# Optimization experiments

Hardware: AMD Instinct MI355X
Metric: run time of the kernel (lower is better)

Reference implementation:

```python
import jax, jax.numpy as jnp
import numpy as np

B, N, D, H = 4, 4096, 1024, 16
HD = D // H


def setup_inputs() -> dict:
    key = jax.random.key(0)
    k_x, k_qkv, k_proj, k_b = jax.random.split(key, 4)
    x = jax.random.normal(k_x, (B, N, D), dtype=jnp.float32)
    # torch nn.Linear weights: (out_features, in_features)
    w_qkv = jax.random.normal(k_qkv, (3 * D, D), dtype=jnp.float32) * (D ** -0.5)
    w_proj = jax.random.normal(k_proj, (D, D), dtype=jnp.float32) * (D ** -0.5)
    b_proj = jax.random.normal(k_b, (D,), dtype=jnp.float32) * 0.01
    return {"x": x, "w_qkv": w_qkv, "w_proj": w_proj, "b_proj": b_proj}


def reference(x, w_qkv, w_proj, b_proj):
    b, n, d = x.shape
    # qkv projection (no bias, qkv_bias=False)
    qkv = x @ w_qkv.T                       # (b, n, 3d)
    qkv = qkv.reshape(b, n, 3, H, HD)
    q, k, v = qkv[:, :, 0], qkv[:, :, 1], qkv[:, :, 2]   # each (b, n, H, HD)
    # Faithful to source: q @ k.transpose(-2,-1) with q,k of shape (b,n,H,HD)
    # -> per-token (H,H) attention across heads, softmax over last (head) axis.
    scale = HD ** -0.5
    attn = jnp.einsum('bnhd,bngd->bnhg', q, k) * scale   # (b, n, H, H)
    attn = jax.nn.softmax(attn, axis=-1)
    o = jnp.einsum('bnhg,bngd->bnhd', attn, v)           # (b, n, H, HD)
    # source: transpose(1,2).reshape(b,n,d) (contiguous copy then reshape)
    o = jnp.swapaxes(o, 1, 2).reshape(b, n, d)
    return o @ w_proj.T + b_proj
```

## Files before the change

kernel.cpp:

```cpp
#include <hip/hip_runtime.h>
#include <hip/hip_bf16.h>
#include <cstdint>
#include <cstddef>

#define NB      4
#define NSEQ    4096
#define DM      1024
#define NTOK    16384
#define QKV_N   3072

typedef __attribute__((ext_vector_type(8))) short short8_t;
typedef __attribute__((ext_vector_type(4))) float f32x4;

static __device__ __forceinline__ unsigned short f2bf(float f) {
    unsigned u = __builtin_bit_cast(unsigned, f);
    u += 0x7fffu + ((u >> 16) & 1u);
    return (unsigned short)(u >> 16);
}

static __device__ __forceinline__ void async16(const void* g, void* l) {
    __builtin_amdgcn_global_load_lds(
        (const __attribute__((address_space(1))) void*)g,
        (__attribute__((address_space(3))) void*)l, 16, 0, 0);
}

__global__ void cvt_f32_bf16(const float* __restrict__ in,
                             unsigned short* __restrict__ out, int n4) {
    int i = blockIdx.x * blockDim.x + threadIdx.x;
    if (i >= n4) return;
    float4 f = ((const float4*)in)[i];
    unsigned lo = (unsigned)f2bf(f.x) | ((unsigned)f2bf(f.y) << 16);
    unsigned hi = (unsigned)f2bf(f.z) | ((unsigned)f2bf(f.w) << 16);
    ((uint2*)out)[i] = make_uint2(lo, hi);
}

template <bool BF16_OUT, bool BIAS>
__global__ __launch_bounds__(256)
void gemm_bt(const unsigned short* __restrict__ A,
             const unsigned short* __restrict__ Bm,
             void* __restrict__ Cv,
             const float* __restrict__ bias,
             int M, int N, int K)
{
    __shared__ alignas(16) unsigned short As[128 * 32];
    __shared__ alignas(16) unsigned short Bs[128 * 32];
    const int t    = threadIdx.x;
    const int lane = t & 63;
    const int quad = lane >> 4;
    const int r16  = lane & 15;
    const int wave = t >> 6;
    const int wm   = (wave >> 1) * 64;
    const int wn   = (wave & 1) * 64;
    const int m0   = blockIdx.y * 128;
    const int n0   = blockIdx.x * 128;

    const int c0 = t, c1 = t + 256;
    const unsigned short* gA0 = A  + (size_t)(m0 + (c0 >> 2)) * K + (c0 & 3) * 8;
    const unsigned short* gA1 = A  + (size_t)(m0 + (c1 >> 2)) * K + (c1 & 3) * 8;
    const unsigned short* gB0 = Bm + (size_t)(n0 + (c0 >> 2)) * K + (c0 & 3) * 8;
    const unsigned short* gB1 = Bm + (size_t)(n0 + (c1 >> 2)) * K + (c1 & 3) * 8;

    f32x4 acc[4][4] = {};

    for (int k0 = 0; k0 < K; k0 += 32) {
        async16(gA0 + k0, As + c0 * 8);
        async16(gA1 + k0, As + c1 * 8);
        async16(gB0 + k0, Bs + c0 * 8);
        async16(gB1 + k0, Bs + c1 * 8);
        __syncthreads();

        short8_t a[4], b[4];
        #pragma unroll
        for (int i = 0; i < 4; ++i)
            a[i] = *(const short8_t*)(As + (wm + i * 16 + r16) * 32 + quad * 8);
        #pragma unroll
        for (int j = 0; j < 4; ++j)
            b[j] = *(const short8_t*)(Bs + (wn + j * 16 + r16) * 32 + quad * 8);
        #pragma unroll
        for (int i = 0; i < 4; ++i)
            #pragma unroll
            for (int j = 0; j < 4; ++j)
                acc[i][j] = __builtin_amdgcn_mfma_f32_16x16x32_bf16(
                    a[i], b[j], acc[i][j], 0, 0, 0);
        __syncthreads();
    }

    #pragma unroll
    for (int i = 0; i < 4; ++i) {
        #pragma unroll
        for (int j = 0; j < 4; ++j) {
            const int col = n0 + wn + j * 16 + r16;
            float bv = 0.f;
            if constexpr (BIAS) bv = bias[col];
            #pragma unroll
            for (int r = 0; r < 4; ++r) {
                const int row = m0 + wm + i * 16 + quad * 4 + r;
                float v = acc[i][j][r] + bv;
                if constexpr (BF16_OUT)
                    ((unsigned short*)Cv)[(size_t)row * N + col] = f2bf(v);
                else
                    ((float*)Cv)[(size_t)row * N + col] = v;
            }
        }
    }
}

__global__ __launch_bounds__(256)
void attn_kernel(const unsigned short* __restrict__ qkv,
                 unsigned short* __restrict__ operm)
{
    __shared__ alignas(16) unsigned short s_qkv[4][QKV_N];
    __shared__ alignas(16) unsigned short s_p[4][256];
    const int t     = threadIdx.x;
    const int lane  = t & 63;
    const int wave  = t >> 6;
    const int quad  = lane >> 4;
    const int r16   = lane & 15;
    const int token = blockIdx.x * 4 + wave;

    {
        const int4* src = (const int4*)(qkv + (size_t)token * QKV_N);
        int4* dst = (int4*)(&s_qkv[wave][0]);
        #pragma unroll
        for (int i = 0; i < 6; ++i) dst[i * 64 + lane] = src[i * 64 + lane];
    }
    __syncthreads();

    const unsigned short* q  = &s_qkv[wave][0];
    const unsigned short* kk = q + 1024;
    const unsigned short* vv = q + 2048;

    f32x4 s = {};
    #pragma unroll
    for (int c = 0; c < 64; c += 32) {
        short8_t aq = *(const short8_t*)(q  + r16 * 64 + c + quad * 8);
        short8_t bk = *(const short8_t*)(kk + r16 * 64 + c + quad * 8);
        s = __builtin_amdgcn_mfma_f32_16x16x32_bf16(aq, bk, s, 0, 0, 0);
    }

    #pragma unroll
    for (int r = 0; r < 4; ++r) {
        float x = s[r] * 0.125f;
        float m = x;
        #pragma unroll
        for (int o = 1; o < 16; o <<= 1) m = fmaxf(m, __shfl_xor(m, o));
        float e = __expf(x - m);
        float su = e;
        #pragma unroll
        for (int o = 1; o < 16; o <<= 1) su += __shfl_xor(su, o);
        s_p[wave][(quad * 4 + r) * 16 + r16] = f2bf(e / su);
    }
    __syncthreads();

    short8_t pa = {};
    if (quad < 2) pa = *(const short8_t*)(&s_p[wave][r16 * 16 + quad * 8]);

    const int b    = token >> 12;
    const int npos = token & 4095;
    const size_t base = (size_t)b * (NSEQ * DM)
                      + (size_t)(npos >> 4) * 1024
                      + (size_t)(npos & 15) * 64;

    #pragma unroll
    for (int j = 0; j < 4; ++j) {
        short8_t vb = {};
        if (quad < 2) {
            #pragma unroll
            for (int e = 0; e < 8; ++e)
                vb[e] = (short)vv[(quad * 8 + e) * 64 + j * 16 + r16];
        }
        f32x4 z = {};
        f32x4 o = __builtin_amdgcn_mfma_f32_16x16x32_bf16(pa, vb, z, 0, 0, 0);
        #pragma unroll
        for (int r = 0; r < 4; ++r) {
            const int h = quad * 4 + r;
            operm[base + (size_t)h * (256 * 1024) + j * 16 + r16] = f2bf(o[r]);
        }
    }
}

extern "C" void kernel_launch(void* const* d_in, const int* in_sizes, int n_in,
                              void* d_out, int out_size, void* d_ws, size_t ws_size,
                              hipStream_t stream)
{
    const float* x      = (const float*)d_in[0];
    const float* w_qkv  = (const float*)d_in[1];
    const float* w_proj = (const float*)d_in[2];
    const float* b_proj = (const float*)d_in[3];
    float* out = (float*)d_out;

    unsigned short* xb     = (unsigned short*)d_ws;
    unsigned short* wqkvb  = xb     + (size_t)16777216;
    unsigned short* wprojb = wqkvb  + (size_t)3145728;
    unsigned short* qkvb   = wprojb + (size_t)1048576;
    unsigned short* opermb = qkvb   + (size_t)50331648;

    cvt_f32_bf16<<<16777216 / 4 / 256, 256, 0, stream>>>(x, xb, 16777216 / 4);
    cvt_f32_bf16<<<3145728 / 4 / 256, 256, 0, stream>>>(w_qkv, wqkvb, 3145728 / 4);
    cvt_f32_bf16<<<1048576 / 4 / 256, 256, 0, stream>>>(w_proj, wprojb, 1048576 / 4);

    dim3 g1(QKV_N / 128, NTOK / 128);
    gemm_bt<true, false><<<g1, 256, 0, stream>>>(xb, wqkvb, qkvb, nullptr,
                                                 NTOK, QKV_N, DM);

    attn_kernel<<<NTOK / 4, 256, 0, stream>>>(qkvb, opermb);

    dim3 g2(DM / 128, NTOK / 128);
    gemm_bt<false, true><<<g2, 256, 0, stream>>>(opermb, wprojb, out, b_proj,
                                                 NTOK, DM, DM);
}
```

Before: 355.7 us.

## Merge conversion launches and coalesce attention loads and stores via LDS

Folds the three fp32-to-bf16 conversion kernels into one launch that picks its source by index range, removing two launches. The attention kernel now fills LDS with async global-to-LDS loads and swaps the divide for a hardware reciprocal. It also stages its outputs in padded shared memory and writes them as 16-byte vectors instead of scattered 2-byte stores. The reciprocal is slightly less precise, and the extra LDS buffer and barrier add a little shared-memory pressure.

```diff
diff --git a/kernel.cpp b/kernel.cpp
--- a/kernel.cpp
+++ b/kernel.cpp
@@ -24,14 +24,22 @@
         (__attribute__((address_space(3))) void*)l, 16, 0, 0);
 }
 
-__global__ void cvt_f32_bf16(const float* __restrict__ in,
-                             unsigned short* __restrict__ out, int n4) {
+__global__ void cvt_all(const float* __restrict__ x,
+                        const float* __restrict__ wqkv,
+                        const float* __restrict__ wproj,
+                        unsigned short* __restrict__ xb,
+                        unsigned short* __restrict__ wqkvb,
+                        unsigned short* __restrict__ wprojb)
+{
     int i = blockIdx.x * blockDim.x + threadIdx.x;
-    if (i >= n4) return;
-    float4 f = ((const float4*)in)[i];
+    const float* src; unsigned short* dst; int off;
+    if (i < 4194304)      { src = x;     dst = xb;     off = i; }
+    else if (i < 4980736) { src = wqkv;  dst = wqkvb;  off = i - 4194304; }
+    else                  { src = wproj; dst = wprojb; off = i - 4980736; }
+    float4 f = ((const float4*)src)[off];
     unsigned lo = (unsigned)f2bf(f.x) | ((unsigned)f2bf(f.y) << 16);
     unsigned hi = (unsigned)f2bf(f.z) | ((unsigned)f2bf(f.w) << 16);
-    ((uint2*)out)[i] = make_uint2(lo, hi);
+    ((uint2*)dst)[off] = make_uint2(lo, hi);
 }
 
 template <bool BF16_OUT, bool BIAS>
@@ -111,6 +119,7 @@
 {
     __shared__ alignas(16) unsigned short s_qkv[4][QKV_N];
     __shared__ alignas(16) unsigned short s_p[4][256];
+    __shared__ alignas(16) unsigned short s_o[4][16 * 72];
     const int t     = threadIdx.x;
     const int lane  = t & 63;
     const int wave  = t >> 6;
@@ -119,10 +128,10 @@
     const int token = blockIdx.x * 4 + wave;
 
     {
-        const int4* src = (const int4*)(qkv + (size_t)token * QKV_N);
-        int4* dst = (int4*)(&s_qkv[wave][0]);
-        #pragma unroll
-        for (int i = 0; i < 6; ++i) dst[i * 64 + lane] = src[i * 64 + lane];
+        const unsigned short* src = qkv + (size_t)token * QKV_N;
+        #pragma unroll
+        for (int i = 0; i < 6; ++i)
+            async16(src + i * 512 + lane * 8, &s_qkv[wave][i * 512 + lane * 8]);
     }
     __syncthreads();
 
@@ -148,19 +157,14 @@
         float su = e;
         #pragma unroll
         for (int o = 1; o < 16; o <<= 1) su += __shfl_xor(su, o);
-        s_p[wave][(quad * 4 + r) * 16 + r16] = f2bf(e / su);
+        s_p[wave][(quad * 4 + r) * 16 + r16] = f2bf(e * __builtin_amdgcn_rcpf(su));
     }
     __syncthreads();
 
     short8_t pa = {};
     if (quad < 2) pa = *(const short8_t*)(&s_p[wave][r16 * 16 + quad * 8]);
 
-    const int b    = token >> 12;
-    const int npos = token & 4095;
-    const size_t base = (size_t)b * (NSEQ * DM)
-                      + (size_t)(npos >> 4) * 1024
-                      + (size_t)(npos & 15) * 64;
-
+    f32x4 o[4];
     #pragma unroll
     for (int j = 0; j < 4; ++j) {
         short8_t vb = {};
@@ -170,12 +174,26 @@
                 vb[e] = (short)vv[(quad * 8 + e) * 64 + j * 16 + r16];
         }
         f32x4 z = {};
-        f32x4 o = __builtin_amdgcn_mfma_f32_16x16x32_bf16(pa, vb, z, 0, 0, 0);
-        #pragma unroll
-        for (int r = 0; r < 4; ++r) {
-            const int h = quad * 4 + r;
-            operm[base + (size_t)h * (256 * 1024) + j * 16 + r16] = f2bf(o[r]);
-        }
+        o[j] = __builtin_amdgcn_mfma_f32_16x16x32_bf16(pa, vb, z, 0, 0, 0);
+    }
+
+    #pragma unroll
+    for (int j = 0; j < 4; ++j)
+        #pragma unroll
+        for (int r = 0; r < 4; ++r)
+            s_o[wave][(quad * 4 + r) * 72 + j * 16 + r16] = f2bf(o[j][r]);
+    __syncthreads();
+
+    const int b    = token >> 12;
+    const int npos = token & 4095;
+    const size_t base = (size_t)b * (NSEQ * DM)
+                      + (size_t)(npos >> 4) * 1024
+                      + (size_t)(npos & 15) * 64;
+    #pragma unroll
+    for (int c = lane; c < 128; c += 64) {
+        const int h = c >> 3, part = c & 7;
+        int4 val = *(const int4*)(&s_o[wave][h * 72 + part * 8]);
+        *(int4*)(operm + base + (size_t)h * (256 * 1024) + part * 8) = val;
     }
 }
 
@@ -195,9 +213,7 @@
     unsigned short* qkvb   = wprojb + (size_t)1048576;
     unsigned short* opermb = qkvb   + (size_t)50331648;
 
-    cvt_f32_bf16<<<16777216 / 4 / 256, 256, 0, stream>>>(x, xb, 16777216 / 4);
-    cvt_f32_bf16<<<3145728 / 4 / 256, 256, 0, stream>>>(w_qkv, wqkvb, 3145728 / 4);
-    cvt_f32_bf16<<<1048576 / 4 / 256, 256, 0, stream>>>(w_proj, wprojb, 1048576 / 4);
+    cvt_all<<<20480, 256, 0, stream>>>(x, w_qkv, w_proj, xb, wqkvb, wprojb);
 
     dim3 g1(QKV_N / 128, NTOK / 128);
     gemm_bt<true, false><<<g1, 256, 0, stream>>>(xb, wqkvb, qkvb, nullptr,
```

After: 353.2 us. About the same (-0.7%).
